# Optimization experiments

Hardware: AMD Instinct MI355X
Metric: run time of the kernel (lower is better)

## Reference

```python
import jax, jax.numpy as jnp
import numpy as np

N, M, K = 8192, 100000, 4096


def setup_inputs() -> dict:
    key = jax.random.key(0)
    k0, k1, k2, k3, k4, k5 = jax.random.split(key, 6)
    origins = jax.random.uniform(k0, (N, 2), dtype=jnp.float32)
    directions = jax.random.uniform(k1, (N, 2), dtype=jnp.float32)
    embeddings = jax.random.uniform(k2, (M, 4), dtype=jnp.float32)
    # Cholesky factors: lower-triangular with strictly positive diagonal
    # (mirrors Encoder.update_parameters: tril + abs(diag)+eps)
    L = jnp.tril(jax.random.uniform(k3, (M, 4, 4), dtype=jnp.float32) * 0.1)
    i4 = jnp.arange(4)
    diag = jnp.abs(L[:, i4, i4]) + 1e-2
    chol = L.at[:, i4, i4].set(diag)
    # labels_embedding in {-1, +1} (Encoder maps 0 -> -1)
    labels = jnp.where(jax.random.randint(k4, (M,), 0, 2) == 0, -1.0, 1.0).astype(jnp.float32)
    idx = jax.random.randint(k5, (K,), 0, M, dtype=jnp.int32)
    return {"origins": origins, "directions": directions, "embeddings": embeddings,
            "chol": chol, "labels": labels, "idx": idx}


def reference(origins, directions, embeddings, chol, labels, idx):
    # Encoder: gather selected gaussians, Sigma = L @ L^T
    mu = embeddings[idx]                                   # [K,4]
    Lsel = chol[idx]                                       # [K,4,4]
    Sigma = jnp.einsum('kij,klj->kil', Lsel, Lsel)         # [K,4,4]
    lab = labels[idx]                                      # [K]
    # Decoder: batched 4x4 inverse + quadratic form + exp + sum + sigmoid
    Sigma_inv = jnp.linalg.inv(Sigma)                      # [K,4,4]
    pos = jnp.concatenate([origins, directions], axis=1)   # [N,4]
    diffs = pos[:, None, :] - mu[None, :, :]               # [N,K,4]
    q = jnp.einsum('nkd,kde,nke->nk', diffs, Sigma_inv, diffs)  # [N,K]
    pdf = lab[None, :] * jnp.exp(-0.5 * q)                 # [N,K]
    prob = jax.nn.sigmoid(jnp.sum(pdf, axis=1))            # [N]
    return prob.reshape(-1, 1)
```

## Files before the change

### kernel.cpp

```cpp
#include <hip/hip_runtime.h>

#define K_TOTAL 4096
#define N_RAYS  8192
#define S_CHUNKS 32
#define CHUNK (K_TOTAL / S_CHUNKS)

__global__ __launch_bounds__(256) void precompute_kernel(
    const float* __restrict__ embeddings,
    const float* __restrict__ chol,
    const float* __restrict__ labels,
    const int*   __restrict__ idx,
    float4*      __restrict__ tab)
{
    int k = blockIdx.x * blockDim.x + threadIdx.x;
    if (k >= K_TOTAL) return;
    int i = idx[k];

    const float* Lp = chol + (size_t)i * 16;
    float l00 = Lp[0];
    float l10 = Lp[4],  l11 = Lp[5];
    float l20 = Lp[8],  l21 = Lp[9],  l22 = Lp[10];
    float l30 = Lp[12], l31 = Lp[13], l32 = Lp[14], l33 = Lp[15];

    float u0 = 1.0f / l00, u1 = 1.0f / l11, u2 = 1.0f / l22, u3 = 1.0f / l33;

    float m00 = u0;
    float m10 = -u1 * (l10 * m00);
    float m11 = u1;
    float m20 = -u2 * (l20 * m00 + l21 * m10);
    float m21 = -u2 * (l21 * m11);
    float m22 = u2;
    float m30 = -u3 * (l30 * m00 + l31 * m10 + l32 * m20);
    float m31 = -u3 * (l31 * m11 + l32 * m21);
    float m32 = -u3 * (l32 * m22);
    float m33 = u3;

    float s00 = m00*m00 + m10*m10 + m20*m20 + m30*m30;
    float s01 = m10*m11 + m20*m21 + m30*m31;
    float s02 = m20*m22 + m30*m32;
    float s03 = m30*m33;
    float s11 = m11*m11 + m21*m21 + m31*m31;
    float s12 = m21*m22 + m31*m32;
    float s13 = m31*m33;
    float s22 = m22*m22 + m32*m32;
    float s23 = m32*m33;
    float s33 = m33*m33;

    const float CD = -0.72134752044448170368f;
    const float CO = -1.44269504088896340736f;

    float4 mu = *(const float4*)(embeddings + (size_t)i * 4);
    float lab = labels[i];

    tab[4*k + 0] = mu;
    tab[4*k + 1] = make_float4(CD*s00, CD*s11, CD*s22, CD*s33);
    tab[4*k + 2] = make_float4(CO*s01, CO*s02, CO*s03, CO*s12);
    tab[4*k + 3] = make_float4(CO*s13, CO*s23, lab, 0.0f);
}

__global__ __launch_bounds__(256) void main_kernel(
    const float*  __restrict__ origins,
    const float*  __restrict__ directions,
    const float4* __restrict__ tab,
    float*        __restrict__ partial)
{
    int n = blockIdx.x * 256 + threadIdx.x;
    int s = blockIdx.y;

    float2 o = ((const float2*)origins)[n];
    float2 d = ((const float2*)directions)[n];
    float p0 = o.x, p1 = o.y, p2 = d.x, p3 = d.y;

    const float4* __restrict__ t = tab + (size_t)s * CHUNK * 4;

    float acc = 0.0f;
    #pragma unroll 4
    for (int k = 0; k < CHUNK; ++k) {
        float4 t0 = t[4*k + 0];
        float4 t1 = t[4*k + 1];
        float4 t2 = t[4*k + 2];
        float4 t3 = t[4*k + 3];
        float d0 = p0 - t0.x;
        float d1 = p1 - t0.y;
        float d2 = p2 - t0.z;
        float d3 = p3 - t0.w;
        float e;
        e = t1.x * (d0 * d0);
        e = fmaf(t1.y, d1 * d1, e);
        e = fmaf(t1.z, d2 * d2, e);
        e = fmaf(t1.w, d3 * d3, e);
        e = fmaf(t2.x, d0 * d1, e);
        e = fmaf(t2.y, d0 * d2, e);
        e = fmaf(t2.z, d0 * d3, e);
        e = fmaf(t2.w, d1 * d2, e);
        e = fmaf(t3.x, d1 * d3, e);
        e = fmaf(t3.y, d2 * d3, e);
        acc = fmaf(t3.z, __builtin_amdgcn_exp2f(e), acc);
    }
    partial[s * N_RAYS + n] = acc;
}

__global__ __launch_bounds__(256) void finish_kernel(
    const float* __restrict__ partial,
    float*       __restrict__ out)
{
    int n = blockIdx.x * 256 + threadIdx.x;
    float sum = 0.0f;
    #pragma unroll
    for (int s = 0; s < S_CHUNKS; ++s)
        sum += partial[s * N_RAYS + n];
    const float L2E = 1.44269504088896340736f;
    out[n] = 1.0f / (1.0f + __builtin_amdgcn_exp2f(-sum * L2E));
}

extern "C" void kernel_launch(void* const* d_in, const int* in_sizes, int n_in,
                              void* d_out, int out_size, void* d_ws, size_t ws_size,
                              hipStream_t stream) {
    const float* origins    = (const float*)d_in[0];
    const float* directions = (const float*)d_in[1];
    const float* embeddings = (const float*)d_in[2];
    const float* chol       = (const float*)d_in[3];
    const float* labels     = (const float*)d_in[4];
    const int*   idx        = (const int*)d_in[5];
    float* out = (float*)d_out;

    float4* tab     = (float4*)d_ws;
    float*  partial = (float*)((char*)d_ws + (size_t)K_TOTAL * 4 * sizeof(float4));

    precompute_kernel<<<dim3(K_TOTAL / 256), dim3(256), 0, stream>>>(
        embeddings, chol, labels, idx, tab);

    main_kernel<<<dim3(N_RAYS / 256, S_CHUNKS), dim3(256), 0, stream>>>(
        origins, directions, tab, partial);

    finish_kernel<<<dim3(N_RAYS / 256), dim3(256), 0, stream>>>(partial, out);
}
```

Before: 96.91 us.

## Use triangular whitening for quadratic form and compute four rays per thread

The precompute now stores the scaled inverse Cholesky factor M = L^{-1} (times sqrt(0.5*log2 e)) and the offset b = -M·mu, so the main loop computes y = M·p + b and sums squares instead of forming differences and ten cross terms. Each thread now handles four rays, reusing each table load across them. The split count rises from 32 to 128 chunks to keep the grid size the same. This cuts FMA count per pair and table-load traffic, but costs more registers and a longer partial-sum reduction in the finish kernel.

```diff
diff --git a/kernel.cpp b/kernel.cpp
--- a/kernel.cpp
+++ b/kernel.cpp
@@ -1,9 +1,14 @@
 #include <hip/hip_runtime.h>
+#include <math.h>
 
 #define K_TOTAL 4096
 #define N_RAYS  8192
-#define S_CHUNKS 32
+#define S_CHUNKS 128
 #define CHUNK (K_TOTAL / S_CHUNKS)
+#define R 4
+#define BLOCK 256
+#define RAYS_PER_BLOCK (BLOCK * R)
+#define NGROUPS (N_RAYS / RAYS_PER_BLOCK)
 
 __global__ __launch_bounds__(256) void precompute_kernel(
     const float* __restrict__ embeddings,
@@ -35,27 +40,22 @@
     float m32 = -u3 * (l32 * m22);
     float m33 = u3;
 
-    float s00 = m00*m00 + m10*m10 + m20*m20 + m30*m30;
-    float s01 = m10*m11 + m20*m21 + m30*m31;
-    float s02 = m20*m22 + m30*m32;
-    float s03 = m30*m33;
-    float s11 = m11*m11 + m21*m21 + m31*m31;
-    float s12 = m21*m22 + m31*m32;
-    float s13 = m31*m33;
-    float s22 = m22*m22 + m32*m32;
-    float s23 = m32*m33;
-    float s33 = m33*m33;
-
-    const float CD = -0.72134752044448170368f;
-    const float CO = -1.44269504088896340736f;
+    const float SC = 0.84932180381996511548f;
+    m00 *= SC; m10 *= SC; m11 *= SC; m20 *= SC; m21 *= SC;
+    m22 *= SC; m30 *= SC; m31 *= SC; m32 *= SC; m33 *= SC;
 
     float4 mu = *(const float4*)(embeddings + (size_t)i * 4);
+    float b0 = -(m00 * mu.x);
+    float b1 = -(m10 * mu.x + m11 * mu.y);
+    float b2 = -(m20 * mu.x + m21 * mu.y + m22 * mu.z);
+    float b3 = -(m30 * mu.x + m31 * mu.y + m32 * mu.z + m33 * mu.w);
+
     float lab = labels[i];
 
-    tab[4*k + 0] = mu;
-    tab[4*k + 1] = make_float4(CD*s00, CD*s11, CD*s22, CD*s33);
-    tab[4*k + 2] = make_float4(CO*s01, CO*s02, CO*s03, CO*s12);
-    tab[4*k + 3] = make_float4(CO*s13, CO*s23, lab, 0.0f);
+    tab[4*k + 0] = make_float4(m00, m10, m11, m20);
+    tab[4*k + 1] = make_float4(m21, m22, m30, m31);
+    tab[4*k + 2] = make_float4(m32, m33, b0, b1);
+    tab[4*k + 3] = make_float4(b2, b3, lab, 0.0f);
 }
 
 __global__ __launch_bounds__(256) void main_kernel(
@@ -64,40 +64,45 @@
     const float4* __restrict__ tab,
     float*        __restrict__ partial)
 {
-    int n = blockIdx.x * 256 + threadIdx.x;
-    int s = blockIdx.y;
+    int tid  = threadIdx.x;
+    int base = blockIdx.x * RAYS_PER_BLOCK + tid;
+    int s    = blockIdx.y;
 
-    float2 o = ((const float2*)origins)[n];
-    float2 d = ((const float2*)directions)[n];
-    float p0 = o.x, p1 = o.y, p2 = d.x, p3 = d.y;
+    float p0[R], p1[R], p2[R], p3[R], acc[R];
+    #pragma unroll
+    for (int r = 0; r < R; ++r) {
+        int n = base + r * BLOCK;
+        float2 o = ((const float2*)origins)[n];
+        float2 d = ((const float2*)directions)[n];
+        p0[r] = o.x; p1[r] = o.y; p2[r] = d.x; p3[r] = d.y;
+        acc[r] = 0.0f;
+    }
 
     const float4* __restrict__ t = tab + (size_t)s * CHUNK * 4;
 
-    float acc = 0.0f;
     #pragma unroll 4
     for (int k = 0; k < CHUNK; ++k) {
         float4 t0 = t[4*k + 0];
         float4 t1 = t[4*k + 1];
         float4 t2 = t[4*k + 2];
         float4 t3 = t[4*k + 3];
-        float d0 = p0 - t0.x;
-        float d1 = p1 - t0.y;
-        float d2 = p2 - t0.z;
-        float d3 = p3 - t0.w;
-        float e;
-        e = t1.x * (d0 * d0);
-        e = fmaf(t1.y, d1 * d1, e);
-        e = fmaf(t1.z, d2 * d2, e);
-        e = fmaf(t1.w, d3 * d3, e);
-        e = fmaf(t2.x, d0 * d1, e);
-        e = fmaf(t2.y, d0 * d2, e);
-        e = fmaf(t2.z, d0 * d3, e);
-        e = fmaf(t2.w, d1 * d2, e);
-        e = fmaf(t3.x, d1 * d3, e);
-        e = fmaf(t3.y, d2 * d3, e);
-        acc = fmaf(t3.z, __builtin_amdgcn_exp2f(e), acc);
+        #pragma unroll
+        for (int r = 0; r < R; ++r) {
+            float y0 = fmaf(t0.x, p0[r], t2.z);
+            float y1 = fmaf(t0.z, p1[r], fmaf(t0.y, p0[r], t2.w));
+            float y2 = fmaf(t1.y, p2[r], fmaf(t1.x, p1[r], fmaf(t0.w, p0[r], t3.x)));
+            float y3 = fmaf(t2.y, p3[r], fmaf(t2.x, p2[r], fmaf(t1.w, p1[r], fmaf(t1.z, p0[r], t3.y))));
+            float sq = y0 * y0;
+            sq = fmaf(y1, y1, sq);
+            sq = fmaf(y2, y2, sq);
+            sq = fmaf(y3, y3, sq);
+            acc[r] = fmaf(t3.z, __builtin_amdgcn_exp2f(-sq), acc[r]);
+        }
     }
-    partial[s * N_RAYS + n] = acc;
+
+    #pragma unroll
+    for (int r = 0; r < R; ++r)
+        partial[(size_t)s * N_RAYS + base + r * BLOCK] = acc[r];
 }
 
 __global__ __launch_bounds__(256) void finish_kernel(
@@ -106,9 +111,9 @@
 {
     int n = blockIdx.x * 256 + threadIdx.x;
     float sum = 0.0f;
-    #pragma unroll
+    #pragma unroll 8
     for (int s = 0; s < S_CHUNKS; ++s)
-        sum += partial[s * N_RAYS + n];
+        sum += partial[(size_t)s * N_RAYS + n];
     const float L2E = 1.44269504088896340736f;
     out[n] = 1.0f / (1.0f + __builtin_amdgcn_exp2f(-sum * L2E));
 }
@@ -130,7 +135,7 @@
     precompute_kernel<<<dim3(K_TOTAL / 256), dim3(256), 0, stream>>>(
         embeddings, chol, labels, idx, tab);
 
-    main_kernel<<<dim3(N_RAYS / 256, S_CHUNKS), dim3(256), 0, stream>>>(
+    main_kernel<<<dim3(NGROUPS, S_CHUNKS), dim3(256), 0, stream>>>(
         origins, directions, tab, partial);
 
     finish_kernel<<<dim3(N_RAYS / 256), dim3(256), 0, stream>>>(partial, out);
```

Result: faster. 93.19 us (-3.8%).
